# Optimization experiments

Measured on AMD Instinct MI355X. Metric: run time of the kernel, lower is better.

The kernel has to match this reference:

```python
import jax, jax.numpy as jnp
import numpy as np

EMB = 512
HEADS = 8
HEAD_DIM = EMB // HEADS


def setup_inputs() -> dict:
    key = jax.random.key(0)
    ks = jax.random.split(key, 8)
    S, B = 2048, 2
    q = jax.random.normal(ks[0], (S, B, EMB), dtype=jnp.float32)
    k = jax.random.normal(ks[1], (S, B, EMB), dtype=jnp.float32)
    v = jax.random.normal(ks[2], (S, B, EMB), dtype=jnp.float32)
    sc = 1.0 / np.sqrt(HEAD_DIM)
    Wq = jax.random.normal(ks[3], (HEAD_DIM, HEAD_DIM), dtype=jnp.float32) * sc
    Wk = jax.random.normal(ks[4], (HEAD_DIM, HEAD_DIM), dtype=jnp.float32) * sc
    Wv = jax.random.normal(ks[5], (HEAD_DIM, HEAD_DIM), dtype=jnp.float32) * sc
    Wfc = jax.random.normal(ks[6], (EMB, EMB), dtype=jnp.float32) * (1.0 / np.sqrt(EMB))
    bfc = jax.random.normal(ks[7], (EMB,), dtype=jnp.float32) * 0.01
    return {"q": q, "k": k, "v": v, "Wq": Wq, "Wk": Wk, "Wv": Wv, "Wfc": Wfc, "bfc": bfc}


def reference(q, k, v, Wq, Wk, Wv, Wfc, bfc):
    query_len, batch, emb = q.shape
    key_len = k.shape[0]
    value_len = v.shape[0]
    # Faithful to the original: plain reshape (NOT transpose) from [S,B,E] -> [B,H,S,D]
    qh = q.reshape(batch, HEADS, query_len, HEAD_DIM)
    kh = k.reshape(batch, HEADS, key_len, HEAD_DIM)
    vh = v.reshape(batch, HEADS, value_len, HEAD_DIM)
    # torch Linear(head_dim, head_dim, bias=False): y = x @ W.T
    Q = qh @ Wq.T
    K = kh @ Wk.T
    V = vh @ Wv.T
    QK = jnp.einsum('bhqd,bhkd->bhqk', Q, K)  # [B,H,S,S] score matrix (memory-bound)
    filt = jax.nn.softmax(QK / np.sqrt(HEAD_DIM).astype(np.float32), axis=3)
    att = jnp.einsum('bhqk,bhkd->bhqd', filt, V)
    att = att.reshape(query_len, batch, emb)
    return att @ Wfc.T + bfc
```

## Files before the change

kernel.cpp:

```cpp
#include <hip/hip_runtime.h>
#include <hip/hip_bf16.h>


typedef __attribute__((ext_vector_type(8))) __bf16 bf16x8;
typedef __attribute__((ext_vector_type(4))) float f32x4;
typedef __attribute__((ext_vector_type(16))) float f32x16;
typedef __attribute__((ext_vector_type(4))) unsigned short u16x4;
typedef __attribute__((ext_vector_type(4))) unsigned int u32x4;
typedef unsigned short u16;
typedef unsigned int u32;

static __device__ __forceinline__ u16 f2bf(float x) {
    u32 u = __float_as_uint(x);
    u += 0x7fff + ((u >> 16) & 1);
    return (u16)(u >> 16);
}
static __device__ __forceinline__ float bf2f(u16 h) {
    return __uint_as_float(((u32)h) << 16);
}
static __device__ __forceinline__ u32 pk2(float lo, float hi) {
    __hip_bfloat162 h2 = __float22bfloat162_rn(make_float2(lo, hi));
    u32 r; __builtin_memcpy(&r, &h2, 4); return r;
}

__global__ __launch_bounds__(256) void proj_kernel(
    const float* __restrict__ q, const float* __restrict__ k, const float* __restrict__ v,
    const float* __restrict__ Wq, const float* __restrict__ Wk, const float* __restrict__ Wv,
    const float* __restrict__ Wfc,
    u16* __restrict__ Qf, u16* __restrict__ Kf, u16* __restrict__ Vf,
    u16* __restrict__ Wb, float* __restrict__ KnSq)
{
    const int mode = blockIdx.z;
    const int t = threadIdx.x;

    if (mode == 3) {
        int i = (blockIdx.x * 256 + t) * 4;
        float4 val = *(const float4*)(Wfc + i);
        uint2 b = { pk2(val.x, val.y), pk2(val.z, val.w) };
        *(uint2*)(Wb + i) = b;
        return;
    }

    const float* A = (mode == 0) ? q : (mode == 1) ? k : v;
    const float* W = (mode == 0) ? Wq : (mode == 1) ? Wk : Wv;
    const float osc = (mode == 0) ? 0.18033688011112042f : 1.0f;

    __shared__ alignas(16) u16 Ash[128 * 88];
    __shared__ alignas(16) u16 Wsh[64 * 88];
    __shared__ float red[128];

    const int m0 = blockIdx.x * 128;
    const int w = t >> 6, l = t & 63;
    const int r16 = l & 15, q4 = l >> 4;

    {
        const float4* A4 = (const float4*)(A + (size_t)m0 * 64);
        const int c4 = t & 15;
        #pragma unroll
        for (int i = 0; i < 8; ++i) {
            int row = (t >> 4) + i * 16;
            float4 val = A4[row * 16 + c4];
            uint2 bb = { pk2(val.x, val.y), pk2(val.z, val.w) };
            *(uint2*)(Ash + row * 88 + c4 * 4) = bb;
        }
        const float4* W4 = (const float4*)W;
        #pragma unroll
        for (int i = 0; i < 4; ++i) {
            int row = (t >> 4) + i * 16;
            float4 val = W4[row * 16 + c4];
            uint2 bb = { pk2(val.x, val.y), pk2(val.z, val.w) };
            *(uint2*)(Wsh + row * 88 + c4 * 4) = bb;
        }
    }
    __syncthreads();

    bf16x8 af[2][2], wf[4][2];
    #pragma unroll
    for (int mc = 0; mc < 2; ++mc)
        #pragma unroll
        for (int kk = 0; kk < 2; ++kk)
            af[mc][kk] = *(const bf16x8*)(Ash + (w * 32 + mc * 16 + r16) * 88 + kk * 32 + q4 * 8);
    #pragma unroll
    for (int nc = 0; nc < 4; ++nc)
        #pragma unroll
        for (int kk = 0; kk < 2; ++kk)
            wf[nc][kk] = *(const bf16x8*)(Wsh + (nc * 16 + r16) * 88 + kk * 32 + q4 * 8);

    f32x4 acc[2][4];
    const f32x4 zero = {0.f, 0.f, 0.f, 0.f};
    #pragma unroll
    for (int mc = 0; mc < 2; ++mc)
        #pragma unroll
        for (int nc = 0; nc < 4; ++nc) {
            acc[mc][nc] = __builtin_amdgcn_mfma_f32_16x16x32_bf16(af[mc][0], wf[nc][0], zero, 0, 0, 0);
            acc[mc][nc] = __builtin_amdgcn_mfma_f32_16x16x32_bf16(af[mc][1], wf[nc][1], acc[mc][nc], 0, 0, 0);
        }

    __syncthreads();

    const int g = m0 >> 11, t0 = (m0 & 2047) >> 6;

    if (mode < 2) {
        #pragma unroll
        for (int mc = 0; mc < 2; ++mc)
            #pragma unroll
            for (int nc = 0; nc < 4; ++nc)
                #pragma unroll
                for (int r = 0; r < 4; ++r)
                    Ash[(w * 32 + mc * 16 + q4 * 4 + r) * 72 + nc * 16 + r16] = f2bf(acc[mc][nc][r] * osc);
        __syncthreads();
        u16* Out = (mode == 0) ? Qf : Kf;
        #pragma unroll
        for (int i = 0; i < 4; ++i) {
            int idx = i * 256 + t;
            int ll = idx & 63;
            int r = idx >> 6;
            int tl = r >> 3, c2 = (r >> 2) & 1, s = r & 3;
            int row = tl * 64 + c2 * 32 + (ll & 31);
            int col = s * 16 + (ll >> 5) * 8;
            u32x4 d = *(const u32x4*)(Ash + row * 72 + col);
            *(u32x4*)(Out + ((size_t)(((g * 32 + t0 + tl) * 2 + c2) * 4 + s) * 64 + ll) * 8) = d;
        }
        if (mode == 1) {
            if (t < 128) {
                float ss = 0.f;
                #pragma unroll
                for (int c = 0; c < 8; ++c) {
                    u32x4 d = *(const u32x4*)(Ash + t * 72 + c * 8);
                    #pragma unroll
                    for (int j = 0; j < 4; ++j) {
                        float lo = bf2f((u16)(d[j] & 0xffff));
                        float hi = bf2f((u16)(d[j] >> 16));
                        ss += lo * lo + hi * hi;
                    }
                }
                red[t] = ss;
            }
            __syncthreads();
            if (t < 64) red[t] = fmaxf(red[t], red[t + 64]);
            __syncthreads();
            if (t < 32) red[t] = fmaxf(red[t], red[t + 32]);
            __syncthreads();
            if (t == 0) {
                float mx = red[0];
                for (int i = 1; i < 32; ++i) mx = fmaxf(mx, red[i]);
                KnSq[blockIdx.x] = mx;
            }
        }
    } else {
        #pragma unroll
        for (int mc = 0; mc < 2; ++mc)
            #pragma unroll
            for (int nc = 0; nc < 4; ++nc)
                #pragma unroll
                for (int r = 0; r < 4; ++r)
                    Ash[(nc * 16 + r16) * 136 + w * 32 + mc * 16 + q4 * 4 + r] = f2bf(acc[mc][nc][r]);
        __syncthreads();
        #pragma unroll
        for (int i = 0; i < 4; ++i) {
            int idx = i * 256 + t;
            int ll = idx & 63;
            int r = idx >> 6;
            int tl = r >> 3, kh = (r >> 2) & 1, dc = (r >> 1) & 1, s2 = r & 1;
            int d = dc * 32 + (ll & 31);
            int keycol = tl * 64 + kh * 32 + s2 * 16 + (ll >> 5) * 8;
            u32x4 val = *(const u32x4*)(Ash + d * 136 + keycol);
            *(u32x4*)(Vf + ((size_t)((((g * 32 + t0 + tl) * 2 + kh) * 2 + dc) * 2 + s2) * 64 + ll) * 8) = val;
        }
    }
}

__global__ __launch_bounds__(512) void flash_kernel(
    const u16* __restrict__ Qf, const u16* __restrict__ Kf,
    const u16* __restrict__ Vf, const float* __restrict__ KnSq,
    u16* __restrict__ Att)
{
    const int bi = blockIdx.x;
    const int g = bi & 15;
    const int qt = bi >> 4;
    const int t = threadIdx.x, w = t >> 6, l = t & 63;
    const int q5 = l & 31, h = l >> 5;
    const int qs = w >> 2;
    const int kq = w & 3;
    const int kh2 = kq & 1, th = kq >> 1;

    __shared__ alignas(16) unsigned char smem[61440];
    u16* const pwRow = (u16*)smem + w * 1280 + q5 * 40;

    const u16* qbase = Qf + ((size_t)(((g * 32 + qt) * 2 + qs) * 4)) * 512 + l * 8;
    const u16* kbase = Kf + ((size_t)(((g * 32 + th * 16) * 2 + kh2) * 4)) * 512 + l * 8;
    const u16* vbase = Vf + ((size_t)((((g * 32 + th * 16) * 2 + kh2) * 2) * 2)) * 512 + l * 8;

    bf16x8 qb[4];
    #pragma unroll
    for (int s = 0; s < 4; ++s) qb[s] = *(const bf16x8*)(qbase + s * 512);

    float m;
    {
        float kss = KnSq[g * 16 + (l & 15)];
        kss = fmaxf(kss, __shfl_xor(kss, 1));
        kss = fmaxf(kss, __shfl_xor(kss, 2));
        kss = fmaxf(kss, __shfl_xor(kss, 4));
        kss = fmaxf(kss, __shfl_xor(kss, 8));
        float ss = 0.f;
        #pragma unroll
        for (int s = 0; s < 4; ++s)
            #pragma unroll
            for (int j = 0; j < 8; ++j) {
                float x = (float)qb[s][j];
                ss += x * x;
            }
        ss += __shfl_xor(ss, 32);
        m = sqrtf(ss * kss) * 1.0002f;
    }

    f32x16 mC, o0, o1, ol;
    #pragma unroll
    for (int r = 0; r < 16; ++r) { mC[r] = -m; o0[r] = 0.f; o1[r] = 0.f; ol[r] = 0.f; }

    const u16 one_bf = 0x3F80;
    bf16x8 ones;
    #pragma unroll
    for (int j = 0; j < 8; ++j) ones[j] = ((const __bf16*)&one_bf)[0];

    bf16x8 ka[4], va[4], kan[4], van[4];
    #pragma unroll
    for (int s = 0; s < 4; ++s) ka[s] = *(const bf16x8*)(kbase + s * 512);
    #pragma unroll
    for (int j = 0; j < 4; ++j) va[j] = *(const bf16x8*)(vbase + j * 512);

    for (int it = 0; it < 16; ++it) {
        const size_t nx = (size_t)((it + 1) & 15) * 4096;
        #pragma unroll
        for (int s = 0; s < 4; ++s) kan[s] = *(const bf16x8*)(kbase + nx + s * 512);
        #pragma unroll
        for (int j = 0; j < 4; ++j) van[j] = *(const bf16x8*)(vbase + nx + j * 512);

        f32x16 s;
        s = __builtin_amdgcn_mfma_f32_32x32x16_bf16(ka[0], qb[0], mC, 0, 0, 0);
        s = __builtin_amdgcn_mfma_f32_32x32x16_bf16(ka[1], qb[1], s, 0, 0, 0);
        s = __builtin_amdgcn_mfma_f32_32x32x16_bf16(ka[2], qb[2], s, 0, 0, 0);
        s = __builtin_amdgcn_mfma_f32_32x32x16_bf16(ka[3], qb[3], s, 0, 0, 0);

        float p[16];
        #pragma unroll
        for (int r = 0; r < 16; ++r) p[r] = exp2f(s[r]);

        #pragma unroll
        for (int u = 0; u < 4; ++u) {
            uint2 dd = { pk2(p[4 * u + 0], p[4 * u + 1]),
                         pk2(p[4 * u + 2], p[4 * u + 3]) };
            *(uint2*)(pwRow + u * 8 + 4 * h) = dd;
        }
        bf16x8 pb0 = *(const bf16x8*)(pwRow + (0 + h) * 8);
        bf16x8 pb1 = *(const bf16x8*)(pwRow + (2 + h) * 8);

        o0 = __builtin_amdgcn_mfma_f32_32x32x16_bf16(va[0], pb0, o0, 0, 0, 0);
        o0 = __builtin_amdgcn_mfma_f32_32x32x16_bf16(va[1], pb1, o0, 0, 0, 0);
        o1 = __builtin_amdgcn_mfma_f32_32x32x16_bf16(va[2], pb0, o1, 0, 0, 0);
        o1 = __builtin_amdgcn_mfma_f32_32x32x16_bf16(va[3], pb1, o1, 0, 0, 0);
        ol = __builtin_amdgcn_mfma_f32_32x32x16_bf16(ones, pb0, ol, 0, 0, 0);
        ol = __builtin_amdgcn_mfma_f32_32x32x16_bf16(ones, pb1, ol, 0, 0, 0);

        #pragma unroll
        for (int s2 = 0; s2 < 4; ++s2) { ka[s2] = kan[s2]; va[s2] = van[s2]; }
    }

    float psq = ol[0];

    float* const Fsh = (float*)smem;
    u16*  const Osh = (u16*)(smem + 52224);

    __syncthreads();
    if (kq != 0) {
        float* fp = Fsh + ((qs * 3) + (kq - 1)) * (64 * 34) + l * 34;
        #pragma unroll
        for (int r = 0; r < 16; ++r) { fp[r] = o0[r]; fp[16 + r] = o1[r]; }
        fp[32] = psq;
    }
    __syncthreads();
    if (kq == 0) {
        float ltot = psq;
        #pragma unroll
        for (int b = 0; b < 3; ++b) {
            const float* fp = Fsh + (qs * 3 + b) * (64 * 34) + l * 34;
            ltot += fp[32];
            #pragma unroll
            for (int r = 0; r < 16; ++r) { o0[r] += fp[r]; o1[r] += fp[16 + r]; }
        }
        float inv = 1.0f / ltot;
        const int qloc = qs * 32 + q5;
        #pragma unroll
        for (int u = 0; u < 4; ++u) {
            uint2 b0 = { pk2(o0[4*u+0] * inv, o0[4*u+1] * inv),
                         pk2(o0[4*u+2] * inv, o0[4*u+3] * inv) };
            *(uint2*)(Osh + qloc * 72 + 8 * u + 4 * h) = b0;
            uint2 b1 = { pk2(o1[4*u+0] * inv, o1[4*u+1] * inv),
                         pk2(o1[4*u+2] * inv, o1[4*u+3] * inv) };
            *(uint2*)(Osh + qloc * 72 + 32 + 8 * u + 4 * h) = b1;
        }
    }
    __syncthreads();
    {
        int row = t >> 3, cb = (t & 7) * 8;
        u16* dst = Att + ((size_t)(g * 2048 + qt * 64 + row)) * 64 + cb;
        *(u32x4*)(dst) = *(const u32x4*)(Osh + row * 72 + cb);
    }
}

__global__ __launch_bounds__(256) void fc_kernel(
    const u16* __restrict__ Att, const u16* __restrict__ Wb,
    const float* __restrict__ bfc, float* __restrict__ out)
{
    __shared__ alignas(16) u16 Ash[2][64 * 64];
    __shared__ alignas(16) u16 Wsh[2][64 * 64];

    const int t = threadIdx.x, w = t >> 6, l = t & 63;
    const int r16 = l & 15, q4 = l >> 4;
    const int r7 = r16 & 7;
    const int m0 = blockIdx.x * 64, n0 = blockIdx.y * 64;

    const int rr = t >> 3, ck = t & 7;
    const int sw0 = (ck ^ (rr & 7)) * 8;
    const int fr0 = (q4 ^ r7) * 8;
    const int fr1 = ((q4 + 4) ^ r7) * 8;

    {
        #pragma unroll
        for (int h = 0; h < 2; ++h) {
            int row = h * 32 + rr;
            *(u32x4*)(&Ash[0][row * 64 + sw0]) = *(const u32x4*)(Att + (size_t)(m0 + row) * 512 + ck * 8);
            *(u32x4*)(&Wsh[0][row * 64 + sw0]) = *(const u32x4*)(Wb + (size_t)(n0 + row) * 512 + ck * 8);
        }
    }
    __syncthreads();

    f32x4 acc[4];
    const f32x4 zero = {0.f, 0.f, 0.f, 0.f};
    #pragma unroll
    for (int nc = 0; nc < 4; ++nc) acc[nc] = zero;

    for (int it = 0; it < 8; ++it) {
        const int cur = it & 1;
        const bool hasn = (it < 7);

        u32x4 anx[2], wnx[2];
        if (hasn) {
            #pragma unroll
            for (int h = 0; h < 2; ++h) {
                int row = h * 32 + rr;
                anx[h] = *(const u32x4*)(Att + (size_t)(m0 + row) * 512 + (it + 1) * 64 + ck * 8);
                wnx[h] = *(const u32x4*)(Wb + (size_t)(n0 + row) * 512 + (it + 1) * 64 + ck * 8);
            }
        }

        bf16x8 af[2], wf[4][2];
        af[0] = *(const bf16x8*)(&Ash[cur][(w * 16 + r16) * 64 + fr0]);
        af[1] = *(const bf16x8*)(&Ash[cur][(w * 16 + r16) * 64 + fr1]);
        #pragma unroll
        for (int nc = 0; nc < 4; ++nc) {
            wf[nc][0] = *(const bf16x8*)(&Wsh[cur][(nc * 16 + r16) * 64 + fr0]);
            wf[nc][1] = *(const bf16x8*)(&Wsh[cur][(nc * 16 + r16) * 64 + fr1]);
        }

        #pragma unroll
        for (int nc = 0; nc < 4; ++nc) {
            acc[nc] = __builtin_amdgcn_mfma_f32_16x16x32_bf16(af[0], wf[nc][0], acc[nc], 0, 0, 0);
            acc[nc] = __builtin_amdgcn_mfma_f32_16x16x32_bf16(af[1], wf[nc][1], acc[nc], 0, 0, 0);
        }

        if (hasn) {
            const int nxt = cur ^ 1;
            #pragma unroll
            for (int h = 0; h < 2; ++h) {
                int row = h * 32 + rr;
                *(u32x4*)(&Ash[nxt][row * 64 + sw0]) = anx[h];
                *(u32x4*)(&Wsh[nxt][row * 64 + sw0]) = wnx[h];
            }
        }
        __syncthreads();
    }

    #pragma unroll
    for (int nc = 0; nc < 4; ++nc) {
        float bb = bfc[n0 + nc * 16 + r16];
        #pragma unroll
        for (int r = 0; r < 4; ++r) {
            int row = m0 + w * 16 + q4 * 4 + r;
            out[(size_t)row * 512 + n0 + nc * 16 + r16] = acc[nc][r] + bb;
        }
    }
}

extern "C" void kernel_launch(void* const* d_in, const int* in_sizes, int n_in,
                              void* d_out, int out_size, void* d_ws, size_t ws_size,
                              hipStream_t stream) {
    (void)in_sizes; (void)n_in; (void)out_size; (void)ws_size;
    const float* q   = (const float*)d_in[0];
    const float* k   = (const float*)d_in[1];
    const float* v   = (const float*)d_in[2];
    const float* Wq  = (const float*)d_in[3];
    const float* Wk  = (const float*)d_in[4];
    const float* Wv  = (const float*)d_in[5];
    const float* Wfc = (const float*)d_in[6];
    const float* bfc = (const float*)d_in[7];
    float* out = (float*)d_out;

    u16* Qf = (u16*)d_ws;
    u16* Kf = Qf + 2097152;
    u16* Vf = Kf + 2097152;
    u16* At = Vf + 2097152;
    u16* Wb = At + 2097152;
    float* KnSq = (float*)((char*)d_ws + 17301504);

    proj_kernel<<<dim3(256, 1, 4), 256, 0, stream>>>(q, k, v, Wq, Wk, Wv, Wfc,
                                                     Qf, Kf, Vf, Wb, KnSq);
    flash_kernel<<<dim3(512), 512, 0, stream>>>(Qf, Kf, Vf, KnSq, At);
    fc_kernel<<<dim3(64, 8), 256, 0, stream>>>(At, Wb, bfc, out);
}
```

Before: 129.2 us.

## Process two query sub-tiles per wave to reuse K/V loads; sum P in VALU

The flash kernel drops from 8 waves to 4 per block, and each wave now handles both 32-row query sub-tiles. Every K/V register fragment is therefore reused for two sets of MFMAs, which halves global K/V traffic per query. The row-sum is now accumulated with scalar adds instead of an extra MFMA against a ones vector. In exchange, register pressure rises (two sets of accumulators and scores), and each block has fewer waves to hide latency.

After: 138.9 us. 1.08x slower.

```diff
diff --git a/kernel.cpp b/kernel.cpp
--- a/kernel.cpp
+++ b/kernel.cpp
@@ -170,7 +170,7 @@
     }
 }
 
-__global__ __launch_bounds__(512) void flash_kernel(
+__global__ __launch_bounds__(256) void flash_kernel(
     const u16* __restrict__ Qf, const u16* __restrict__ Kf,
     const u16* __restrict__ Vf, const float* __restrict__ KnSq,
     u16* __restrict__ Att)
@@ -180,48 +180,57 @@
     const int qt = bi >> 4;
     const int t = threadIdx.x, w = t >> 6, l = t & 63;
     const int q5 = l & 31, h = l >> 5;
-    const int qs = w >> 2;
-    const int kq = w & 3;
+    const int kq = w;
     const int kh2 = kq & 1, th = kq >> 1;
 
     __shared__ alignas(16) unsigned char smem[61440];
-    u16* const pwRow = (u16*)smem + w * 1280 + q5 * 40;
-
-    const u16* qbase = Qf + ((size_t)(((g * 32 + qt) * 2 + qs) * 4)) * 512 + l * 8;
+    u16* const pwA = (u16*)smem + (w * 2 + 0) * 1280 + q5 * 40;
+    u16* const pwB = (u16*)smem + (w * 2 + 1) * 1280 + q5 * 40;
+
+    const u16* qbase = Qf + ((size_t)((g * 32 + qt) * 2 * 4)) * 512 + l * 8;
     const u16* kbase = Kf + ((size_t)(((g * 32 + th * 16) * 2 + kh2) * 4)) * 512 + l * 8;
     const u16* vbase = Vf + ((size_t)((((g * 32 + th * 16) * 2 + kh2) * 2) * 2)) * 512 + l * 8;
 
-    bf16x8 qb[4];
-    #pragma unroll
-    for (int s = 0; s < 4; ++s) qb[s] = *(const bf16x8*)(qbase + s * 512);
-
-    float m;
+    bf16x8 qa[4], qc[4];
+    #pragma unroll
+    for (int s = 0; s < 4; ++s) {
+        qa[s] = *(const bf16x8*)(qbase + s * 512);
+        qc[s] = *(const bf16x8*)(qbase + 2048 + s * 512);
+    }
+
+    float kss;
     {
-        float kss = KnSq[g * 16 + (l & 15)];
+        kss = KnSq[g * 16 + (l & 15)];
         kss = fmaxf(kss, __shfl_xor(kss, 1));
         kss = fmaxf(kss, __shfl_xor(kss, 2));
         kss = fmaxf(kss, __shfl_xor(kss, 4));
         kss = fmaxf(kss, __shfl_xor(kss, 8));
-        float ss = 0.f;
+    }
+    float m0v, m1v;
+    {
+        float ss0 = 0.f, ss1 = 0.f;
         #pragma unroll
         for (int s = 0; s < 4; ++s)
             #pragma unroll
             for (int j = 0; j < 8; ++j) {
-                float x = (float)qb[s][j];
-                ss += x * x;
-            }
-        ss += __shfl_xor(ss, 32);
-        m = sqrtf(ss * kss) * 1.0002f;
-    }
-
-    f32x16 mC, o0, o1, ol;
-    #pragma unroll
-    for (int r = 0; r < 16; ++r) { mC[r] = -m; o0[r] = 0.f; o1[r] = 0.f; ol[r] = 0.f; }
-
-    const u16 one_bf = 0x3F80;
-    bf16x8 ones;
-    #pragma unroll
-    for (int j = 0; j < 8; ++j) ones[j] = ((const __bf16*)&one_bf)[0];
+                float x0 = (float)qa[s][j];
+                float x1 = (float)qc[s][j];
+                ss0 += x0 * x0;
+                ss1 += x1 * x1;
+            }
+        ss0 += __shfl_xor(ss0, 32);
+        ss1 += __shfl_xor(ss1, 32);
+        m0v = sqrtf(ss0 * kss) * 1.0002f;
+        m1v = sqrtf(ss1 * kss) * 1.0002f;
+    }
+
+    f32x16 mC0, mC1, o0a, o1a, o0b, o1b;
+    #pragma unroll
+    for (int r = 0; r < 16; ++r) {
+        mC0[r] = -m0v; mC1[r] = -m1v;
+        o0a[r] = 0.f; o1a[r] = 0.f; o0b[r] = 0.f; o1b[r] = 0.f;
+    }
+    float ls0 = 0.f, ls1 = 0.f;
 
     bf16x8 ka[4], va[4], kan[4], van[4];
     #pragma unroll
@@ -236,75 +245,120 @@
         #pragma unroll
         for (int j = 0; j < 4; ++j) van[j] = *(const bf16x8*)(vbase + nx + j * 512);
 
-        f32x16 s;
-        s = __builtin_amdgcn_mfma_f32_32x32x16_bf16(ka[0], qb[0], mC, 0, 0, 0);
-        s = __builtin_amdgcn_mfma_f32_32x32x16_bf16(ka[1], qb[1], s, 0, 0, 0);
-        s = __builtin_amdgcn_mfma_f32_32x32x16_bf16(ka[2], qb[2], s, 0, 0, 0);
-        s = __builtin_amdgcn_mfma_f32_32x32x16_bf16(ka[3], qb[3], s, 0, 0, 0);
-
-        float p[16];
-        #pragma unroll
-        for (int r = 0; r < 16; ++r) p[r] = exp2f(s[r]);
+        f32x16 s0, s1;
+        s0 = __builtin_amdgcn_mfma_f32_32x32x16_bf16(ka[0], qa[0], mC0, 0, 0, 0);
+        s1 = __builtin_amdgcn_mfma_f32_32x32x16_bf16(ka[0], qc[0], mC1, 0, 0, 0);
+        s0 = __builtin_amdgcn_mfma_f32_32x32x16_bf16(ka[1], qa[1], s0, 0, 0, 0);
+        s1 = __builtin_amdgcn_mfma_f32_32x32x16_bf16(ka[1], qc[1], s1, 0, 0, 0);
+        s0 = __builtin_amdgcn_mfma_f32_32x32x16_bf16(ka[2], qa[2], s0, 0, 0, 0);
+        s1 = __builtin_amdgcn_mfma_f32_32x32x16_bf16(ka[2], qc[2], s1, 0, 0, 0);
+        s0 = __builtin_amdgcn_mfma_f32_32x32x16_bf16(ka[3], qa[3], s0, 0, 0, 0);
+        s1 = __builtin_amdgcn_mfma_f32_32x32x16_bf16(ka[3], qc[3], s1, 0, 0, 0);
+
+        float p0[16], p1[16];
+        #pragma unroll
+        for (int r = 0; r < 16; ++r) {
+            p0[r] = exp2f(s0[r]);
+            p1[r] = exp2f(s1[r]);
+            ls0 += p0[r];
+            ls1 += p1[r];
+        }
 
         #pragma unroll
         for (int u = 0; u < 4; ++u) {
-            uint2 dd = { pk2(p[4 * u + 0], p[4 * u + 1]),
-                         pk2(p[4 * u + 2], p[4 * u + 3]) };
-            *(uint2*)(pwRow + u * 8 + 4 * h) = dd;
-        }
-        bf16x8 pb0 = *(const bf16x8*)(pwRow + (0 + h) * 8);
-        bf16x8 pb1 = *(const bf16x8*)(pwRow + (2 + h) * 8);
-
-        o0 = __builtin_amdgcn_mfma_f32_32x32x16_bf16(va[0], pb0, o0, 0, 0, 0);
-        o0 = __builtin_amdgcn_mfma_f32_32x32x16_bf16(va[1], pb1, o0, 0, 0, 0);
-        o1 = __builtin_amdgcn_mfma_f32_32x32x16_bf16(va[2], pb0, o1, 0, 0, 0);
-        o1 = __builtin_amdgcn_mfma_f32_32x32x16_bf16(va[3], pb1, o1, 0, 0, 0);
-        ol = __builtin_amdgcn_mfma_f32_32x32x16_bf16(ones, pb0, ol, 0, 0, 0);
-        ol = __builtin_amdgcn_mfma_f32_32x32x16_bf16(ones, pb1, ol, 0, 0, 0);
+            uint2 d0 = { pk2(p0[4 * u + 0], p0[4 * u + 1]),
+                         pk2(p0[4 * u + 2], p0[4 * u + 3]) };
+            *(uint2*)(pwA + u * 8 + 4 * h) = d0;
+            uint2 d1 = { pk2(p1[4 * u + 0], p1[4 * u + 1]),
+                         pk2(p1[4 * u + 2], p1[4 * u + 3]) };
+            *(uint2*)(pwB + u * 8 + 4 * h) = d1;
+        }
+        bf16x8 pa0 = *(const bf16x8*)(pwA + (0 + h) * 8);
+        bf16x8 pa1 = *(const bf16x8*)(pwA + (2 + h) * 8);
+        bf16x8 pb0 = *(const bf16x8*)(pwB + (0 + h) * 8);
+        bf16x8 pb1 = *(const bf16x8*)(pwB + (2 + h) * 8);
+
+        o0a = __builtin_amdgcn_mfma_f32_32x32x16_bf16(va[0], pa0, o0a, 0, 0, 0);
+        o0b = __builtin_amdgcn_mfma_f32_32x32x16_bf16(va[0], pb0, o0b, 0, 0, 0);
+        o0a = __builtin_amdgcn_mfma_f32_32x32x16_bf16(va[1], pa1, o0a, 0, 0, 0);
+        o0b = __builtin_amdgcn_mfma_f32_32x32x16_bf16(va[1], pb1, o0b, 0, 0, 0);
+        o1a = __builtin_amdgcn_mfma_f32_32x32x16_bf16(va[2], pa0, o1a, 0, 0, 0);
+        o1b = __builtin_amdgcn_mfma_f32_32x32x16_bf16(va[2], pb0, o1b, 0, 0, 0);
+        o1a = __builtin_amdgcn_mfma_f32_32x32x16_bf16(va[3], pa1, o1a, 0, 0, 0);
+        o1b = __builtin_amdgcn_mfma_f32_32x32x16_bf16(va[3], pb1, o1b, 0, 0, 0);
 
         #pragma unroll
         for (int s2 = 0; s2 < 4; ++s2) { ka[s2] = kan[s2]; va[s2] = van[s2]; }
     }
 
-    float psq = ol[0];
+    float psq0 = ls0 + __shfl_xor(ls0, 32);
+    float psq1 = ls1 + __shfl_xor(ls1, 32);
 
     float* const Fsh = (float*)smem;
     u16*  const Osh = (u16*)(smem + 52224);
 
     __syncthreads();
     if (kq != 0) {
-        float* fp = Fsh + ((qs * 3) + (kq - 1)) * (64 * 34) + l * 34;
-        #pragma unroll
-        for (int r = 0; r < 16; ++r) { fp[r] = o0[r]; fp[16 + r] = o1[r]; }
-        fp[32] = psq;
+        float* f0 = Fsh + (0 * 3 + (kq - 1)) * (64 * 34) + l * 34;
+        float* f1 = Fsh + (1 * 3 + (kq - 1)) * (64 * 34) + l * 34;
+        #pragma unroll
+        for (int r = 0; r < 16; ++r) {
+            f0[r] = o0a[r]; f0[16 + r] = o1a[r];
+            f1[r] = o0b[r]; f1[16 + r] = o1b[r];
+        }
+        f0[32] = psq0;
+        f1[32] = psq1;
     }
     __syncthreads();
     if (kq == 0) {
-        float ltot = psq;
-        #pragma unroll
-        for (int b = 0; b < 3; ++b) {
-            const float* fp = Fsh + (qs * 3 + b) * (64 * 34) + l * 34;
-            ltot += fp[32];
-            #pragma unroll
-            for (int r = 0; r < 16; ++r) { o0[r] += fp[r]; o1[r] += fp[16 + r]; }
-        }
-        float inv = 1.0f / ltot;
-        const int qloc = qs * 32 + q5;
-        #pragma unroll
-        for (int u = 0; u < 4; ++u) {
-            uint2 b0 = { pk2(o0[4*u+0] * inv, o0[4*u+1] * inv),
-                         pk2(o0[4*u+2] * inv, o0[4*u+3] * inv) };
-            *(uint2*)(Osh + qloc * 72 + 8 * u + 4 * h) = b0;
-            uint2 b1 = { pk2(o1[4*u+0] * inv, o1[4*u+1] * inv),
-                         pk2(o1[4*u+2] * inv, o1[4*u+3] * inv) };
-            *(uint2*)(Osh + qloc * 72 + 32 + 8 * u + 4 * h) = b1;
+        {
+            float ltot = psq0;
+            #pragma unroll
+            for (int b = 0; b < 3; ++b) {
+                const float* fp = Fsh + (0 * 3 + b) * (64 * 34) + l * 34;
+                ltot += fp[32];
+                #pragma unroll
+                for (int r = 0; r < 16; ++r) { o0a[r] += fp[r]; o1a[r] += fp[16 + r]; }
+            }
+            float inv = 1.0f / ltot;
+            #pragma unroll
+            for (int u = 0; u < 4; ++u) {
+                uint2 b0 = { pk2(o0a[4*u+0] * inv, o0a[4*u+1] * inv),
+                             pk2(o0a[4*u+2] * inv, o0a[4*u+3] * inv) };
+                *(uint2*)(Osh + q5 * 72 + 8 * u + 4 * h) = b0;
+                uint2 b1 = { pk2(o1a[4*u+0] * inv, o1a[4*u+1] * inv),
+                             pk2(o1a[4*u+2] * inv, o1a[4*u+3] * inv) };
+                *(uint2*)(Osh + q5 * 72 + 32 + 8 * u + 4 * h) = b1;
+            }
+        }
+        {
+            float ltot = psq1;
+            #pragma unroll
+            for (int b = 0; b < 3; ++b) {
+                const float* fp = Fsh + (1 * 3 + b) * (64 * 34) + l * 34;
+                ltot += fp[32];
+                #pragma unroll
+                for (int r = 0; r < 16; ++r) { o0b[r] += fp[r]; o1b[r] += fp[16 + r]; }
+            }
+            float inv = 1.0f / ltot;
+            const int qloc = 32 + q5;
+            #pragma unroll
+            for (int u = 0; u < 4; ++u) {
+                uint2 b0 = { pk2(o0b[4*u+0] * inv, o0b[4*u+1] * inv),
+                             pk2(o0b[4*u+2] * inv, o0b[4*u+3] * inv) };
+                *(uint2*)(Osh + qloc * 72 + 8 * u + 4 * h) = b0;
+                uint2 b1 = { pk2(o1b[4*u+0] * inv, o1b[4*u+1] * inv),
+                             pk2(o1b[4*u+2] * inv, o1b[4*u+3] * inv) };
+                *(uint2*)(Osh + qloc * 72 + 32 + 8 * u + 4 * h) = b1;
+            }
         }
     }
     __syncthreads();
     {
-        int row = t >> 3, cb = (t & 7) * 8;
+        int row = t >> 2, cb = (t & 3) * 16;
         u16* dst = Att + ((size_t)(g * 2048 + qt * 64 + row)) * 64 + cb;
-        *(u32x4*)(dst) = *(const u32x4*)(Osh + row * 72 + cb);
+        *(u32x4*)(dst)     = *(const u32x4*)(Osh + row * 72 + cb);
+        *(u32x4*)(dst + 8) = *(const u32x4*)(Osh + row * 72 + cb + 8);
     }
 }
 
@@ -415,6 +469,6 @@
 
     proj_kernel<<<dim3(256, 1, 4), 256, 0, stream>>>(q, k, v, Wq, Wk, Wv, Wfc,
                                                      Qf, Kf, Vf, Wb, KnSq);
-    flash_kernel<<<dim3(512), 512, 0, stream>>>(Qf, Kf, Vf, KnSq, At);
+    flash_kernel<<<dim3(512), 256, 0, stream>>>(Qf, Kf, Vf, KnSq, At);
     fc_kernel<<<dim3(64, 8), 256, 0, stream>>>(At, Wb, bfc, out);
 }
```
